# Kernel optimization log

Measured on AMD Instinct MI355X. Metric: run time of the kernel, lower is better.

## Reference

```python
import jax, jax.numpy as jnp
import numpy as np

C = 128          # hidden_channels
H = 8            # num_heads
D = C // H       # head dim = 16
OUT = 64         # out_channels
L = 2            # num_layers
NN = (30000, 60000, 6000)                 # poi, road, region node counts
NE = (200000, 300000, 200000, 100000)     # edges per edge type
ETS = ((0, 1), (1, 1), (1, 2), (2, 0))    # (src_type, dst_type) per edge type


def setup_inputs():
    key = jax.random.key(0)
    ks = iter(jax.random.split(key, 40))
    s = 1.0 / np.sqrt(C)
    sd = 1.0 / np.sqrt(D)
    inp = {}
    inp['x_poi'] = jax.random.normal(next(ks), (NN[0], C), jnp.float32)
    inp['x_road'] = jax.random.normal(next(ks), (NN[1], C), jnp.float32)
    inp['x_region'] = jax.random.normal(next(ks), (NN[2], C), jnp.float32)
    for et, (si, di) in enumerate(ETS):
        inp[f'e{et}_src'] = jax.random.randint(next(ks), (NE[et],), 0, NN[si], jnp.int32)
        inp[f'e{et}_dst'] = jax.random.randint(next(ks), (NE[et],), 0, NN[di], jnp.int32)
    # per-node-type input projection
    inp['lin_w'] = jax.random.normal(next(ks), (3, C, C), jnp.float32) * s
    inp['lin_b'] = jax.random.normal(next(ks), (3, C), jnp.float32) * 0.01
    # per-layer, per-node-type K/Q/V and output projections
    for nm in ('kw', 'qw', 'vw', 'aw'):
        inp[nm] = jax.random.normal(next(ks), (L, 3, C, C), jnp.float32) * s
    for nm in ('kb', 'qb', 'vb', 'ab'):
        inp[nm] = jax.random.normal(next(ks), (L, 3, C), jnp.float32) * 0.01
    # per-layer, per-edge-type relation matrices and priors
    inp['a_rel'] = jax.random.normal(next(ks), (L, 4, H, D, D), jnp.float32) * sd
    inp['m_rel'] = jax.random.normal(next(ks), (L, 4, H, D, D), jnp.float32) * sd
    inp['p_rel'] = jnp.ones((L, 4, H), jnp.float32)
    inp['skip'] = jnp.ones((L, 3), jnp.float32)
    inp['out_w'] = jax.random.normal(next(ks), (C, OUT), jnp.float32) * s
    inp['out_b'] = jnp.zeros((OUT,), jnp.float32)
    return inp


def _seg_softmax(alpha, dst, n):
    amax = jax.lax.stop_gradient(jax.ops.segment_max(alpha, dst, num_segments=n))
    ex = jnp.exp(alpha - amax[dst])
    den = jax.ops.segment_sum(ex, dst, num_segments=n)
    return ex / (den[dst] + 1e-16)


def _hgt_forward(xs, edges, lin_w, lin_b, kw, kb, qw, qb, vw, vb, aw, ab,
                 a_rel, m_rel, p_rel, skip, out_w, out_b):
    # per-node-type input linear + relu
    xs = [jax.nn.relu(xs[i] @ lin_w[i] + lin_b[i]) for i in range(3)]
    scale = 1.0 / np.sqrt(D)
    for l in range(L):
        k = [(xs[i] @ kw[l, i] + kb[l, i]).reshape(-1, H, D) for i in range(3)]
        q = [(xs[i] @ qw[l, i] + qb[l, i]).reshape(-1, H, D) for i in range(3)]
        v = [(xs[i] @ vw[l, i] + vb[l, i]).reshape(-1, H, D) for i in range(3)]
        agg = [jnp.zeros((NN[i], H, D), xs[i].dtype) for i in range(3)]
        for et, (si, di) in enumerate(ETS):
            src, dst = edges[et]
            n = NN[di]
            ke = jnp.einsum('ehd,hdf->ehf', k[si][src], a_rel[l, et])   # [E,H,D]
            alpha = jnp.einsum('ehd,ehd->eh', q[di][dst], ke) * p_rel[l, et] * scale
            alpha = _seg_softmax(alpha, dst, n)                          # [E,H]
            m = jnp.einsum('ehd,hdf->ehf', v[si][src], m_rel[l, et])    # [E,H,D]
            agg[di] = agg[di] + jax.ops.segment_sum(m * alpha[..., None], dst, num_segments=n)
        new_xs = []
        for i in range(3):
            o = jax.nn.gelu(agg[i].reshape(-1, C)) @ aw[l, i] + ab[l, i]
            beta = jax.nn.sigmoid(skip[l, i])
            o = beta * o + (1.0 - beta) * xs[i]
            new_xs.append(jax.nn.relu(o))  # HGT applies activation after each conv
        xs = new_xs
    return (xs[0] @ out_w + out_b, xs[1] @ out_w + out_b, xs[2] @ out_w + out_b)


def reference(x_poi, x_road, x_region,
              e0_src, e0_dst, e1_src, e1_dst, e2_src, e2_dst, e3_src, e3_dst,
              lin_w, lin_b, kw, kb, qw, qb, vw, vb, aw, ab,
              a_rel, m_rel, p_rel, skip, out_w, out_b):
    edges = ((e0_src, e0_dst), (e1_src, e1_dst), (e2_src, e2_dst), (e3_src, e3_dst))
    return _hgt_forward([x_poi, x_road, x_region], edges,
                        lin_w, lin_b, kw, kb, qw, qb, vw, vb, aw, ab,
                        a_rel, m_rel, p_rel, skip, out_w, out_b)
```

## Files before the change

kernel.cpp:

```cpp
#include <hip/hip_runtime.h>
#include <cstddef>
#include <cstdint>


typedef __attribute__((ext_vector_type(8))) short short8;
typedef __attribute__((ext_vector_type(4))) float floatx4;

__device__ __forceinline__ float gelu_fast(float x) {
    float u = 1.5957691216057308f * x * (1.0f + 0.044715f * x * x);
    return x / (1.0f + __expf(-u));
}

__device__ __forceinline__ unsigned short f2bf(float f) {
    unsigned u = __float_as_uint(f);
    u += 0x7fffu + ((u >> 16) & 1);
    return (unsigned short)(u >> 16);
}

__device__ __forceinline__ float bf2f(unsigned short h) {
    return __uint_as_float((unsigned)h << 16);
}

__device__ __forceinline__ void up8(uint4 u, float* f) {
    f[0] = __uint_as_float(u.x << 16); f[1] = __uint_as_float(u.x & 0xffff0000u);
    f[2] = __uint_as_float(u.y << 16); f[3] = __uint_as_float(u.y & 0xffff0000u);
    f[4] = __uint_as_float(u.z << 16); f[5] = __uint_as_float(u.z & 0xffff0000u);
    f[6] = __uint_as_float(u.w << 16); f[7] = __uint_as_float(u.w & 0xffff0000u);
}

__device__ __forceinline__ uint4 pk8(const float* f) {
    uint4 u;
    u.x = (unsigned)f2bf(f[0]) | ((unsigned)f2bf(f[1]) << 16);
    u.y = (unsigned)f2bf(f[2]) | ((unsigned)f2bf(f[3]) << 16);
    u.z = (unsigned)f2bf(f[4]) | ((unsigned)f2bf(f[5]) << 16);
    u.w = (unsigned)f2bf(f[6]) | ((unsigned)f2bf(f[7]) << 16);
    return u;
}

__global__ __launch_bounds__(256) void gemm_proj(
    const unsigned short* __restrict__ Abf,
    const unsigned short* __restrict__ Wt,
    const float* __restrict__ bias,
    unsigned short* __restrict__ outbf, int ldo, int Nrows, int cpb, int nct)
{
    const int wave = threadIdx.x >> 6, lane = threadIdx.x & 63;
    const int quad = lane >> 4, l16 = lane & 15;
    const int rowStart = (blockIdx.y * 4 + wave) * 32;
    if (rowStart >= Nrows) return;
    short8 Afr[2][4];
    #pragma unroll
    for (int rt = 0; rt < 2; ++rt) {
        int m = rowStart + rt * 16 + l16;
        const unsigned short* ap = Abf + (size_t)((m < Nrows) ? m : 0) * 128 + quad * 8;
        #pragma unroll
        for (int kc = 0; kc < 4; ++kc)
            Afr[rt][kc] = *(const short8*)(ap + kc * 32);
    }
    int ct1 = blockIdx.x * cpb + cpb;
    if (ct1 > nct) ct1 = nct;
    for (int ct = blockIdx.x * cpb; ct < ct1; ++ct) {
        int colBase = ct * 64;
        const unsigned short* wp = Wt + (size_t)(colBase + l16) * 128 + quad * 8;
        short8 B[4][4];
        #pragma unroll
        for (int c = 0; c < 4; ++c)
            #pragma unroll
            for (int kc = 0; kc < 4; ++kc)
                B[c][kc] = *(const short8*)(wp + (size_t)c * 2048 + kc * 32);
        floatx4 acc[2][4] = {{{0,0,0,0},{0,0,0,0},{0,0,0,0},{0,0,0,0}},
                             {{0,0,0,0},{0,0,0,0},{0,0,0,0},{0,0,0,0}}};
        #pragma unroll
        for (int kc = 0; kc < 4; ++kc)
            #pragma unroll
            for (int c = 0; c < 4; ++c) {
                acc[0][c] = __builtin_amdgcn_mfma_f32_16x16x32_bf16(Afr[0][kc], B[c][kc], acc[0][c], 0, 0, 0);
                acc[1][c] = __builtin_amdgcn_mfma_f32_16x16x32_bf16(Afr[1][kc], B[c][kc], acc[1][c], 0, 0, 0);
            }
        #pragma unroll
        for (int rt = 0; rt < 2; ++rt) {
            int row0 = rowStart + rt * 16 + quad * 4;
            #pragma unroll
            for (int c = 0; c < 4; ++c) {
                int col = colBase + c * 16 + l16;
                float bv = bias[col];
                #pragma unroll
                for (int r = 0; r < 4; ++r) {
                    int row = row0 + r;
                    if (row < Nrows)
                        outbf[(size_t)row * ldo + col] = f2bf(acc[rt][c][r] + bv);
                }
            }
        }
    }
}

template<bool AF32, bool GIN, bool SKIP>
__global__ __launch_bounds__(256) void gemm_node(
    const void* __restrict__ a0v, const void* __restrict__ a1v, const void* __restrict__ a2v,
    const unsigned short* __restrict__ WtB, const float* __restrict__ biasB,
    const unsigned short* __restrict__ xoldB, const float* __restrict__ skipB,
    unsigned short* __restrict__ outB)
{
    const int TN[3]   = {30000, 60000, 6000};
    const int TOFF[3] = {0, 30000, 90000};
    int by = blockIdx.x;
    int t  = (by < 469) ? 0 : (by < 1407) ? 1 : 2;
    int lb = by - ((t == 0) ? 0 : (t == 1) ? 469 : 1407);
    int Nrows = TN[t];
    const void* av = (t == 0) ? a0v : (t == 1) ? a1v : a2v;
    const unsigned short* Wt = WtB + (size_t)t * 16384;
    const float* bias = biasB + t * 128;
    const unsigned short* xold = xoldB + (size_t)TOFF[t] * 128;
    unsigned short* out = outB + (size_t)TOFF[t] * 128;
    const int wave = threadIdx.x >> 6, lane = threadIdx.x & 63;
    const int quad = lane >> 4, l16 = lane & 15;
    const int rowStart = (lb * 4 + wave) * 16;
    if (rowStart >= Nrows) return;
    int m = rowStart + l16;
    size_t base = (size_t)((m < Nrows) ? m : 0) * 128 + quad * 8;
    short8 Afr[4];
    #pragma unroll
    for (int kc = 0; kc < 4; ++kc) {
        if (AF32) {
            const float* ap = (const float*)av + base;
            float4 f0 = *(const float4*)(ap + kc * 32);
            float4 f1 = *(const float4*)(ap + kc * 32 + 4);
            float af[8] = {f0.x, f0.y, f0.z, f0.w, f1.x, f1.y, f1.z, f1.w};
            short8 a;
            #pragma unroll
            for (int i = 0; i < 8; ++i) a[i] = (short)f2bf(af[i]);
            Afr[kc] = a;
        } else if (GIN) {
            const unsigned short* ap = (const unsigned short*)av + base;
            short8 a8 = *(const short8*)(ap + kc * 32);
            short8 a;
            #pragma unroll
            for (int i = 0; i < 8; ++i)
                a[i] = (short)f2bf(gelu_fast(bf2f((unsigned short)a8[i])));
            Afr[kc] = a;
        } else {
            const unsigned short* ap = (const unsigned short*)av + base;
            Afr[kc] = *(const short8*)(ap + kc * 32);
        }
    }
    float beta = 0.f, omb = 0.f;
    if (SKIP) { beta = 1.0f / (1.0f + __expf(-skipB[t])); omb = 1.0f - beta; }
    int row0 = rowStart + quad * 4;
    #pragma unroll
    for (int ct = 0; ct < 2; ++ct) {
        int colBase = ct * 64;
        const unsigned short* wp = Wt + (size_t)(colBase + l16) * 128 + quad * 8;
        #pragma unroll
        for (int c = 0; c < 4; ++c) {
            floatx4 acc = {0, 0, 0, 0};
            #pragma unroll
            for (int kc = 0; kc < 4; ++kc) {
                short8 B = *(const short8*)(wp + (size_t)c * 2048 + kc * 32);
                acc = __builtin_amdgcn_mfma_f32_16x16x32_bf16(Afr[kc], B, acc, 0, 0, 0);
            }
            int col = colBase + c * 16 + l16;
            float bv = bias[col];
            #pragma unroll
            for (int r = 0; r < 4; ++r) {
                int row = row0 + r;
                if (row < Nrows) {
                    float o = acc[r] + bv;
                    if (SKIP) o = beta * o + omb * bf2f(xold[(size_t)row * 128 + col]);
                    o = fmaxf(o, 0.f);
                    out[(size_t)row * 128 + col] = f2bf(o);
                }
            }
        }
    }
}

__global__ __launch_bounds__(256) void gemm_out(
    const unsigned short* __restrict__ Abf,
    const unsigned short* __restrict__ Wt,
    const float* __restrict__ bias,
    float* __restrict__ out, int Nrows)
{
    const int wave = threadIdx.x >> 6, lane = threadIdx.x & 63;
    const int quad = lane >> 4, l16 = lane & 15;
    const int rowBase = (blockIdx.x * 4 + wave) * 16;
    if (rowBase >= Nrows) return;
    const unsigned short* wp = Wt + (size_t)l16 * 128 + quad * 8;
    int m = rowBase + l16;
    const unsigned short* ap = Abf + (size_t)((m < Nrows) ? m : 0) * 128 + quad * 8;
    short8 Afr[4];
    #pragma unroll
    for (int kc = 0; kc < 4; ++kc) Afr[kc] = *(const short8*)(ap + kc * 32);
    int row0 = rowBase + quad * 4;
    #pragma unroll
    for (int c = 0; c < 4; ++c) {
        floatx4 acc = {0, 0, 0, 0};
        #pragma unroll
        for (int kc = 0; kc < 4; ++kc) {
            short8 B = *(const short8*)(wp + (size_t)c * 2048 + kc * 32);
            acc = __builtin_amdgcn_mfma_f32_16x16x32_bf16(Afr[kc], B, acc, 0, 0, 0);
        }
        int col = c * 16 + l16;
        float bv = bias[col];
        #pragma unroll
        for (int r = 0; r < 4; ++r) {
            int row = row0 + r;
            if (row < Nrows)
                out[(size_t)row * 64 + col] = acc[r] + bv;
        }
    }
}

__global__ __launch_bounds__(128) void prep_qpack(
    const float* __restrict__ qw, const float* __restrict__ qb,
    unsigned short* __restrict__ Wpack, float* __restrict__ bpack)
{
    const int pre[3] = {0, 49152, 131072};
    const int preB[3] = {0, 384, 1024};
    int n = threadIdx.x, k = blockIdx.x, t = blockIdx.y, l = blockIdx.z;
    unsigned short* Wp = Wpack + (size_t)l * 180224 + pre[t];
    Wp[(size_t)n * 128 + k] = f2bf(qw[(size_t)(l * 3 + t) * 16384 + (size_t)k * 128 + n]);
    if (k == 0) bpack[l * 1408 + preB[t] + n] = qb[(l * 3 + t) * 128 + n];
}

__global__ __launch_bounds__(128) void fold_rel_pack(
    const float* __restrict__ kw, const float* __restrict__ kb,
    const float* __restrict__ vw, const float* __restrict__ vb,
    const float* __restrict__ a_rel, const float* __restrict__ m_rel,
    unsigned short* __restrict__ Wpack, float* __restrict__ bpack)
{
    const int SIv[4] = {0, 1, 1, 2};
    const int SLOT[4] = {0, 0, 1, 0};
    const int pre[3] = {0, 49152, 131072};
    const int preB[3] = {0, 384, 1024};
    int hf = threadIdx.x, h = hf >> 4, f = hf & 15;
    int c = blockIdx.x, et = blockIdx.y, l = blockIdx.z;
    int si = SIv[et];
    const float* kwp  = kw + (size_t)(l * 3 + si) * 16384;
    const float* vwp  = vw + (size_t)(l * 3 + si) * 16384;
    const float* kbp  = kb + (size_t)(l * 3 + si) * 128;
    const float* vbp  = vb + (size_t)(l * 3 + si) * 128;
    const float* arel = a_rel + (size_t)(l * 4 + et) * 2048;
    const float* mrel = m_rel + (size_t)(l * 4 + et) * 2048;
    float sk = 0.f, sv = 0.f;
    #pragma unroll
    for (int d = 0; d < 16; ++d) {
        float ar = arel[(h * 16 + d) * 16 + f];
        float mr = mrel[(h * 16 + d) * 16 + f];
        sk = fmaf(kwp[c * 128 + h * 16 + d], ar, sk);
        sv = fmaf(vwp[c * 128 + h * 16 + d], mr, sv);
    }
    int rowoff = 128 + 256 * SLOT[et];
    unsigned short* Wp = Wpack + (size_t)l * 180224 + pre[si];
    Wp[(size_t)(rowoff + hf) * 128 + c]       = f2bf(sk);
    Wp[(size_t)(rowoff + 128 + hf) * 128 + c] = f2bf(sv);
    if (c == 0) {
        float bk = 0.f, bvv = 0.f;
        #pragma unroll
        for (int d = 0; d < 16; ++d) {
            bk  = fmaf(kbp[h * 16 + d], arel[(h * 16 + d) * 16 + f], bk);
            bvv = fmaf(vbp[h * 16 + d], mrel[(h * 16 + d) * 16 + f], bvv);
        }
        float* bp = bpack + l * 1408 + preB[si];
        bp[rowoff + hf]       = bk;
        bp[rowoff + 128 + hf] = bvv;
    }
}

__global__ __launch_bounds__(128) void prep_w9(
    const float* __restrict__ lin_w, const float* __restrict__ aw,
    unsigned short* __restrict__ lwt, unsigned short* __restrict__ awt)
{
    int n = threadIdx.x, k = blockIdx.x, mi = blockIdx.y;
    const float* w; unsigned short* wt; int m;
    if (mi < 3) { w = lin_w; wt = lwt; m = mi; }
    else        { w = aw;    wt = awt; m = mi - 3; }
    wt[(size_t)m * 16384 + (size_t)n * 128 + k] =
        f2bf(w[(size_t)m * 16384 + (size_t)k * 128 + n]);
}

__global__ __launch_bounds__(64) void prep_owt(
    const float* __restrict__ ow, unsigned short* __restrict__ owt)
{
    int n = threadIdx.x, k = blockIdx.x;
    owt[(size_t)n * 128 + k] = f2bf(ow[(size_t)k * 64 + n]);
}

__global__ __launch_bounds__(256) void hist_all(
    const int* __restrict__ d0, const int* __restrict__ d1,
    const int* __restrict__ d2, const int* __restrict__ d3,
    int* __restrict__ deg4)
{
    const int Ev[4] = {200000, 300000, 200000, 100000};
    int et = blockIdx.y;
    int e = blockIdx.x * 256 + threadIdx.x;
    if (e >= Ev[et]) return;
    const int* d = et == 0 ? d0 : et == 1 ? d1 : et == 2 ? d2 : d3;
    atomicAdd(&deg4[et * 60000 + d[e]], 1);
}

__global__ __launch_bounds__(256) void scan_tile_all(
    const int* __restrict__ deg4,
    int* __restrict__ r0, int* __restrict__ r1, int* __restrict__ r2, int* __restrict__ r3,
    int* __restrict__ tsum4)
{
    const int Ndv[4] = {60000, 60000, 6000, 30000};
    __shared__ int ls[256];
    int et = blockIdx.y;
    int n = Ndv[et];
    const int* deg = deg4 + et * 60000;
    int* rowptr = et == 0 ? r0 : et == 1 ? r1 : et == 2 ? r2 : r3;
    int b = blockIdx.x, tid = threadIdx.x;
    int base = b * 1024 + tid * 4;
    int v0 = 0, v1 = 0, v2 = 0, v3 = 0;
    if (base + 3 < n) {
        int4 t = *(const int4*)(deg + base);
        v0 = t.x; v1 = t.y; v2 = t.z; v3 = t.w;
    } else {
        if (base + 0 < n) v0 = deg[base + 0];
        if (base + 1 < n) v1 = deg[base + 1];
        if (base + 2 < n) v2 = deg[base + 2];
        if (base + 3 < n) v3 = deg[base + 3];
    }
    int s = v0 + v1 + v2 + v3;
    ls[tid] = s;
    __syncthreads();
    #pragma unroll
    for (int off = 1; off < 256; off <<= 1) {
        int t = (tid >= off) ? ls[tid - off] : 0;
        __syncthreads();
        ls[tid] += t;
        __syncthreads();
    }
    int run = ls[tid] - s;
    int o0 = run; run += v0;
    int o1 = run; run += v1;
    int o2 = run; run += v2;
    int o3 = run;
    if (base + 3 < n) {
        *(int4*)(rowptr + base) = make_int4(o0, o1, o2, o3);
    } else {
        if (base + 0 < n) rowptr[base + 0] = o0;
        if (base + 1 < n) rowptr[base + 1] = o1;
        if (base + 2 < n) rowptr[base + 2] = o2;
    }
    if (tid == 255) tsum4[et * 64 + b] = ls[255];
}

__global__ __launch_bounds__(64) void scan_tsum_all(
    int* __restrict__ tsum4,
    int* __restrict__ r0, int* __restrict__ r1, int* __restrict__ r2, int* __restrict__ r3)
{
    const int Ndv[4] = {60000, 60000, 6000, 30000};
    int et = blockIdx.x;
    int n = Ndv[et];
    int nt = (n + 1023) >> 10;
    int* tileSum = tsum4 + et * 64;
    int* rowptr = et == 0 ? r0 : et == 1 ? r1 : et == 2 ? r2 : r3;
    int tid = threadIdx.x;
    int v = (tid < nt) ? tileSum[tid] : 0;
    int orig = v;
    #pragma unroll
    for (int off = 1; off < 64; off <<= 1) {
        int t = __shfl_up(v, off);
        if (tid >= off) v += t;
    }
    if (tid < nt) tileSum[tid] = v - orig;
    if (tid == nt - 1) rowptr[n] = v;
}

__global__ __launch_bounds__(256) void scan_add_all(
    int* __restrict__ r0, int* __restrict__ r1, int* __restrict__ r2, int* __restrict__ r3,
    const int* __restrict__ tsum4)
{
    const int Ndv[4] = {60000, 60000, 6000, 30000};
    int et = blockIdx.y;
    int n = Ndv[et];
    int* rowptr = et == 0 ? r0 : et == 1 ? r1 : et == 2 ? r2 : r3;
    int i = blockIdx.x * 256 + threadIdx.x;
    if (i < n) rowptr[i] += tsum4[et * 64 + (i >> 10)];
}

__global__ __launch_bounds__(256) void fill_all(
    const int* __restrict__ s0, const int* __restrict__ d0,
    const int* __restrict__ s1, const int* __restrict__ d1,
    const int* __restrict__ s2, const int* __restrict__ d2,
    const int* __restrict__ s3, const int* __restrict__ d3,
    const int* __restrict__ r0, const int* __restrict__ r1,
    const int* __restrict__ r2, const int* __restrict__ r3,
    int* __restrict__ deg4,
    int* __restrict__ c0, int* __restrict__ c1, int* __restrict__ c2, int* __restrict__ c3)
{
    const int Ev[4] = {200000, 300000, 200000, 100000};
    int et = blockIdx.y;
    int e = blockIdx.x * 256 + threadIdx.x;
    if (e >= Ev[et]) return;
    const int* src = et == 0 ? s0 : et == 1 ? s1 : et == 2 ? s2 : s3;
    const int* dst = et == 0 ? d0 : et == 1 ? d1 : et == 2 ? d2 : d3;
    const int* rowptr = et == 0 ? r0 : et == 1 ? r1 : et == 2 ? r2 : r3;
    int* csr = et == 0 ? c0 : et == 1 ? c1 : et == 2 ? c2 : c3;
    int d = dst[e];
    int pos = atomicAdd(&deg4[et * 60000 + d], 1);
    csr[rowptr[d] + pos] = src[e];
}

__device__ __forceinline__ void attn_run(
    const int* __restrict__ csr, int beg, int end,
    const unsigned short* __restrict__ kbase, int ld,
    const float* qf, float ph, float& m, float& l, float* o)
{
    if (beg >= end) return;
    int s = csr[beg];
    for (int j = beg; j < end; ++j) {
        int sn = (j + 1 < end) ? csr[j + 1] : 0;
        const uint4* kp = (const uint4*)(kbase + (size_t)s * ld);
        uint4 ku0 = kp[0], ku1 = kp[1];
        uint4 vu0 = kp[16], vu1 = kp[17];
        float kf[16], vf[16];
        up8(ku0, kf); up8(ku1, kf + 8);
        up8(vu0, vf); up8(vu1, vf + 8);
        float a = 0.f;
        #pragma unroll
        for (int i = 0; i < 16; ++i) a = fmaf(qf[i], kf[i], a);
        a *= ph;
        float mn = fmaxf(m, a);
        float sc = __expf(m - mn);
        float w  = __expf(a - mn);
        l = l * sc + w;
        #pragma unroll
        for (int i = 0; i < 16; ++i) o[i] = o[i] * sc + w * vf[i];
        m = mn; s = sn;
    }
}

__global__ __launch_bounds__(256) void agg_all(
    const int* __restrict__ rp0, const int* __restrict__ cs0,
    const int* __restrict__ rp1, const int* __restrict__ cs1,
    const int* __restrict__ rp2, const int* __restrict__ cs2,
    const int* __restrict__ rp3, const int* __restrict__ cs3,
    const unsigned short* __restrict__ P0, const unsigned short* __restrict__ P1,
    const unsigned short* __restrict__ P2,
    const float* __restrict__ prl,
    unsigned short* __restrict__ num)
{
    int gb = blockIdx.x, tid = threadIdx.x;
    float qf[16], o[16], r[16];
    if (gb < 1875) {
        int t = gb * 256 + tid;
        int node = t >> 3, h = t & 7;
        const uint4* qp = (const uint4*)(P1 + (size_t)node * 640 + h * 16);
        up8(qp[0], qf); up8(qp[1], qf + 8);
        float m0 = -INFINITY, l0 = 0.f;
        #pragma unroll
        for (int i = 0; i < 16; ++i) o[i] = 0.f;
        attn_run(cs0, rp0[node], rp0[node + 1], P0 + 128 + h * 16, 384,
                 qf, prl[h] * 0.25f, m0, l0, o);
        float i0 = 1.f / (l0 + 1e-16f);
        #pragma unroll
        for (int i = 0; i < 16; ++i) { r[i] = i0 * o[i]; o[i] = 0.f; }
        float m1 = -INFINITY, l1 = 0.f;
        attn_run(cs1, rp1[node], rp1[node + 1], P1 + 128 + h * 16, 640,
                 qf, prl[8 + h] * 0.25f, m1, l1, o);
        float i1 = 1.f / (l1 + 1e-16f);
        #pragma unroll
        for (int i = 0; i < 16; ++i) r[i] += i1 * o[i];
        uint4* np = (uint4*)(num + (size_t)(30000 + node) * 128 + h * 16);
        np[0] = pk8(r); np[1] = pk8(r + 8);
    } else if (gb < 2250) {
        int t = (gb - 1875) * 256 + tid;
        int node = t >> 4, h = t & 7, half = (t >> 3) & 1;
        int beg = rp2[node], end = rp2[node + 1];
        int mid = beg + ((end - beg + 1) >> 1);
        if (half == 0) end = mid; else beg = mid;
        const uint4* qp = (const uint4*)(P2 + (size_t)node * 384 + h * 16);
        up8(qp[0], qf); up8(qp[1], qf + 8);
        float m = -INFINITY, l = 0.f;
        #pragma unroll
        for (int i = 0; i < 16; ++i) o[i] = 0.f;
        attn_run(cs2, beg, end, P1 + 384 + h * 16, 640,
                 qf, prl[16 + h] * 0.25f, m, l, o);
        float mp = __shfl_xor(m, 8);
        float lp = __shfl_xor(l, 8);
        float mn = fmaxf(m, mp);
        float sc  = (l  > 0.f) ? __expf(m  - mn) : 0.f;
        float scp = (lp > 0.f) ? __expf(mp - mn) : 0.f;
        l = l * sc + lp * scp;
        #pragma unroll
        for (int i = 0; i < 16; ++i) {
            float op = __shfl_xor(o[i], 8);
            o[i] = o[i] * sc + op * scp;
        }
        if (half) return;
        float inv = 1.f / (l + 1e-16f);
        #pragma unroll
        for (int i = 0; i < 16; ++i) r[i] = inv * o[i];
        uint4* np = (uint4*)(num + (size_t)(90000 + node) * 128 + h * 16);
        np[0] = pk8(r); np[1] = pk8(r + 8);
    } else {
        int t = (gb - 2250) * 256 + tid;
        if (t >= 240000) return;
        int node = t >> 3, h = t & 7;
        const uint4* qp = (const uint4*)(P0 + (size_t)node * 384 + h * 16);
        up8(qp[0], qf); up8(qp[1], qf + 8);
        float m = -INFINITY, l = 0.f;
        #pragma unroll
        for (int i = 0; i < 16; ++i) o[i] = 0.f;
        attn_run(cs3, rp3[node], rp3[node + 1], P2 + 128 + h * 16, 384,
                 qf, prl[24 + h] * 0.25f, m, l, o);
        float inv = 1.f / (l + 1e-16f);
        #pragma unroll
        for (int i = 0; i < 16; ++i) r[i] = inv * o[i];
        uint4* np = (uint4*)(num + (size_t)node * 128 + h * 16);
        np[0] = pk8(r); np[1] = pk8(r + 8);
    }
}

extern "C" void kernel_launch(void* const* d_in, const int* in_sizes, int n_in,
                              void* d_out, int out_size, void* d_ws, size_t ws_size,
                              hipStream_t stream)
{
    (void)in_sizes; (void)n_in; (void)out_size; (void)ws_size;

    const float* xin[3] = {(const float*)d_in[0], (const float*)d_in[1], (const float*)d_in[2]};
    const int* esrc[4] = {(const int*)d_in[3], (const int*)d_in[5], (const int*)d_in[7], (const int*)d_in[9]};
    const int* edst[4] = {(const int*)d_in[4], (const int*)d_in[6], (const int*)d_in[8], (const int*)d_in[10]};
    const float* lin_w = (const float*)d_in[11];
    const float* lin_b = (const float*)d_in[12];
    const float* kw = (const float*)d_in[13];
    const float* qw = (const float*)d_in[14];
    const float* vw = (const float*)d_in[15];
    const float* aw = (const float*)d_in[16];
    const float* kb = (const float*)d_in[17];
    const float* qb = (const float*)d_in[18];
    const float* vb = (const float*)d_in[19];
    const float* ab = (const float*)d_in[20];
    const float* a_rel = (const float*)d_in[21];
    const float* m_rel = (const float*)d_in[22];
    const float* p_rel = (const float*)d_in[23];
    const float* skip  = (const float*)d_in[24];
    const float* out_w = (const float*)d_in[25];
    const float* out_b = (const float*)d_in[26];

    float* ws = (float*)d_ws;
    unsigned short* num   = (unsigned short*)ws;
    unsigned short* xs_bf = (unsigned short*)(ws + 6144000);
    unsigned short* proj  = (unsigned short*)(ws + 12288000);
    unsigned short* Wpack = (unsigned short*)(ws + 38400000);
    unsigned short* lwt   = (unsigned short*)(ws + 38580224);
    unsigned short* awt   = (unsigned short*)(ws + 38604800);
    unsigned short* owt   = (unsigned short*)(ws + 38653952);
    float*          bpack = ws + 38658048;
    int*            deg4  = (int*)(ws + 38660864);
    int*            tsum4 = (int*)(ws + 38900864);
    int* rp[4];
    rp[0] = (int*)(ws + 38901120);
    rp[1] = (int*)(ws + 38961128);
    rp[2] = (int*)(ws + 39021136);
    rp[3] = (int*)(ws + 39027144);
    int* cs[4];
    cs[0] = (int*)(ws + 39057152);
    cs[1] = (int*)(ws + 39257152);
    cs[2] = (int*)(ws + 39557152);
    cs[3] = (int*)(ws + 39757152);

    const int NNv[3] = {30000, 60000, 6000};
    const int OFF[3] = {0, 30000, 90000};
    const int NCOLS[3] = {384, 640, 384};
    unsigned short* P[3];
    P[0] = proj;
    P[1] = proj + (size_t)30000 * 384;
    P[2] = proj + (size_t)30000 * 384 + (size_t)60000 * 640;

    dim3 blk(256);

    hipMemsetAsync(deg4, 0, 960000, stream);
    hist_all<<<dim3(1172, 4), blk, 0, stream>>>(edst[0], edst[1], edst[2], edst[3], deg4);
    scan_tile_all<<<dim3(59, 4), blk, 0, stream>>>(deg4, rp[0], rp[1], rp[2], rp[3], tsum4);
    scan_tsum_all<<<dim3(4), dim3(64), 0, stream>>>(tsum4, rp[0], rp[1], rp[2], rp[3]);
    scan_add_all<<<dim3(235, 4), blk, 0, stream>>>(rp[0], rp[1], rp[2], rp[3], tsum4);
    hipMemsetAsync(deg4, 0, 960000, stream);
    fill_all<<<dim3(1172, 4), blk, 0, stream>>>(
        esrc[0], edst[0], esrc[1], edst[1], esrc[2], edst[2], esrc[3], edst[3],
        rp[0], rp[1], rp[2], rp[3], deg4, cs[0], cs[1], cs[2], cs[3]);

    prep_qpack<<<dim3(128, 3, 2), dim3(128), 0, stream>>>(qw, qb, Wpack, bpack);
    fold_rel_pack<<<dim3(128, 4, 2), dim3(128), 0, stream>>>(
        kw, kb, vw, vb, a_rel, m_rel, Wpack, bpack);
    prep_w9<<<dim3(128, 9), dim3(128), 0, stream>>>(lin_w, aw, lwt, awt);
    prep_owt<<<dim3(128), dim3(64), 0, stream>>>(out_w, owt);

    gemm_node<true, false, false><<<dim3(1501), blk, 0, stream>>>(
        xin[0], xin[1], xin[2], lwt, lin_b, nullptr, nullptr, xs_bf);

    for (int l = 0; l < 2; ++l) {
        const int CPB[3] = {3, 5, 2};
        const int XG[3]  = {2, 2, 3};
        for (int i = 0; i < 3; ++i) {
            dim3 g(XG[i], (NNv[i] + 127) / 128);
            gemm_proj<<<g, blk, 0, stream>>>(
                xs_bf + (size_t)OFF[i] * 128,
                Wpack + (size_t)l * 180224 + (i == 0 ? 0 : i == 1 ? 49152 : 131072),
                bpack + l * 1408 + (i == 0 ? 0 : i == 1 ? 384 : 1024),
                P[i], NCOLS[i], NNv[i], CPB[i], NCOLS[i] / 64);
        }

        agg_all<<<dim3(3188), blk, 0, stream>>>(
            rp[0], cs[0], rp[1], cs[1], rp[2], cs[2], rp[3], cs[3],
            P[0], P[1], P[2], p_rel + (size_t)l * 32, num);

        gemm_node<false, true, true><<<dim3(1501), blk, 0, stream>>>(
            num, num + (size_t)30000 * 128, num + (size_t)90000 * 128,
            awt + (size_t)l * 3 * 16384, ab + (size_t)l * 3 * 128,
            xs_bf, skip + l * 3, xs_bf);
    }

    gemm_out<<<dim3(1500), blk, 0, stream>>>(
        xs_bf, owt, out_b, (float*)d_out, 96000);
}
```

Measured before the change: 669.7 us.

## Fuse projection GEMMs, prefetch next edge, lazy softmax rescale, 4-way split region

The three per-node-type projection GEMM launches become one launch that maps block indices to node types. The attention inner loop now prefetches the next source row's K/V before computing the current edge. It also replaces the per-edge online-softmax rescale with a lazy rescale that only fires when the running max grows by more than 8. Region-destination aggregation is split four ways per node instead of two, merged with two shuffle rounds. These aim to cut launch overhead, hide gather latency and reduce exp work, at the cost of more registers and a lazy-max accuracy tradeoff.

```diff
diff --git a/kernel.cpp b/kernel.cpp
--- a/kernel.cpp
+++ b/kernel.cpp
@@ -37,15 +37,37 @@
     return u;
 }
 
-__global__ __launch_bounds__(256) void gemm_proj(
-    const unsigned short* __restrict__ Abf,
-    const unsigned short* __restrict__ Wt,
-    const float* __restrict__ bias,
-    unsigned short* __restrict__ outbf, int ldo, int Nrows, int cpb, int nct)
-{
+__global__ __launch_bounds__(256) void gemm_proj_all(
+    const unsigned short* __restrict__ xs_bf,
+    const unsigned short* __restrict__ Wl,
+    const float* __restrict__ bl,
+    unsigned short* __restrict__ proj)
+{
+    const int    NN_[3]  = {30000, 60000, 6000};
+    const int    OFFr[3] = {0, 30000, 90000};
+    const int    WOFF[3] = {0, 49152, 131072};
+    const int    BOFF[3] = {0, 384, 1024};
+    const size_t POFF[3] = {0, 11520000u, 49920000u};
+    const int    LDO[3]  = {384, 640, 384};
+    const int    CPBv[3] = {3, 5, 2};
+
+    int by = blockIdx.x, t, lb;
+    if (by < 938)       { t = 1; lb = by; }
+    else if (by < 1408) { t = 0; lb = by - 938; }
+    else                { t = 2; lb = by - 1408; }
+    int bx, byy;
+    if (t == 2) { byy = lb / 3; bx = lb - byy * 3; }
+    else        { bx = lb & 1; byy = lb >> 1; }
+
+    const unsigned short* Abf = xs_bf + (size_t)OFFr[t] * 128;
+    const unsigned short* Wt  = Wl + WOFF[t];
+    const float* bias = bl + BOFF[t];
+    unsigned short* outbf = proj + POFF[t];
+    const int ldo = LDO[t], Nrows = NN_[t], cpb = CPBv[t], nct = ldo >> 6;
+
     const int wave = threadIdx.x >> 6, lane = threadIdx.x & 63;
     const int quad = lane >> 4, l16 = lane & 15;
-    const int rowStart = (blockIdx.y * 4 + wave) * 32;
+    const int rowStart = (byy * 4 + wave) * 32;
     if (rowStart >= Nrows) return;
     short8 Afr[2][4];
     #pragma unroll
@@ -56,9 +78,9 @@
         for (int kc = 0; kc < 4; ++kc)
             Afr[rt][kc] = *(const short8*)(ap + kc * 32);
     }
-    int ct1 = blockIdx.x * cpb + cpb;
+    int ct1 = bx * cpb + cpb;
     if (ct1 > nct) ct1 = nct;
-    for (int ct = blockIdx.x * cpb; ct < ct1; ++ct) {
+    for (int ct = bx * cpb; ct < ct1; ++ct) {
         int colBase = ct * 64;
         const unsigned short* wp = Wt + (size_t)(colBase + l16) * 128 + quad * 8;
         short8 B[4][4];
@@ -410,11 +432,16 @@
 {
     if (beg >= end) return;
     int s = csr[beg];
+    const uint4* kp = (const uint4*)(kbase + (size_t)s * ld);
+    uint4 ku0 = kp[0], ku1 = kp[1];
+    uint4 vu0 = kp[16], vu1 = kp[17];
     for (int j = beg; j < end; ++j) {
-        int sn = (j + 1 < end) ? csr[j + 1] : 0;
-        const uint4* kp = (const uint4*)(kbase + (size_t)s * ld);
-        uint4 ku0 = kp[0], ku1 = kp[1];
-        uint4 vu0 = kp[16], vu1 = kp[17];
+        uint4 nk0 = ku0, nk1 = ku1, nv0 = vu0, nv1 = vu1;
+        if (j + 1 < end) {
+            int sn = csr[j + 1];
+            const uint4* np = (const uint4*)(kbase + (size_t)sn * ld);
+            nk0 = np[0]; nk1 = np[1]; nv0 = np[16]; nv1 = np[17];
+        }
         float kf[16], vf[16];
         up8(ku0, kf); up8(ku1, kf + 8);
         up8(vu0, vf); up8(vu1, vf + 8);
@@ -422,13 +449,19 @@
         #pragma unroll
         for (int i = 0; i < 16; ++i) a = fmaf(qf[i], kf[i], a);
         a *= ph;
-        float mn = fmaxf(m, a);
-        float sc = __expf(m - mn);
-        float w  = __expf(a - mn);
-        l = l * sc + w;
-        #pragma unroll
-        for (int i = 0; i < 16; ++i) o[i] = o[i] * sc + w * vf[i];
-        m = mn; s = sn;
+        float d = a - m;
+        if (d > 8.f) {
+            float sc = __expf(-d);
+            l *= sc;
+            #pragma unroll
+            for (int i = 0; i < 16; ++i) o[i] *= sc;
+            m = a; d = 0.f;
+        }
+        float w = __expf(d);
+        l += w;
+        #pragma unroll
+        for (int i = 0; i < 16; ++i) o[i] = fmaf(w, vf[i], o[i]);
+        ku0 = nk0; ku1 = nk1; vu0 = nv0; vu1 = nv1;
     }
 }
 
@@ -465,12 +498,13 @@
         for (int i = 0; i < 16; ++i) r[i] += i1 * o[i];
         uint4* np = (uint4*)(num + (size_t)(30000 + node) * 128 + h * 16);
         np[0] = pk8(r); np[1] = pk8(r + 8);
-    } else if (gb < 2250) {
+    } else if (gb < 2625) {
         int t = (gb - 1875) * 256 + tid;
-        int node = t >> 4, h = t & 7, half = (t >> 3) & 1;
-        int beg = rp2[node], end = rp2[node + 1];
-        int mid = beg + ((end - beg + 1) >> 1);
-        if (half == 0) end = mid; else beg = mid;
+        int node = t >> 5, h = t & 7, sub = (t >> 3) & 3;
+        int beg0 = rp2[node], end0 = rp2[node + 1];
+        int n = end0 - beg0;
+        int beg = beg0 + ((n * sub) >> 2);
+        int end = beg0 + ((n * (sub + 1)) >> 2);
         const uint4* qp = (const uint4*)(P2 + (size_t)node * 384 + h * 16);
         up8(qp[0], qf); up8(qp[1], qf + 8);
         float m = -INFINITY, l = 0.f;
@@ -478,25 +512,29 @@
         for (int i = 0; i < 16; ++i) o[i] = 0.f;
         attn_run(cs2, beg, end, P1 + 384 + h * 16, 640,
                  qf, prl[16 + h] * 0.25f, m, l, o);
-        float mp = __shfl_xor(m, 8);
-        float lp = __shfl_xor(l, 8);
-        float mn = fmaxf(m, mp);
-        float sc  = (l  > 0.f) ? __expf(m  - mn) : 0.f;
-        float scp = (lp > 0.f) ? __expf(mp - mn) : 0.f;
-        l = l * sc + lp * scp;
-        #pragma unroll
-        for (int i = 0; i < 16; ++i) {
-            float op = __shfl_xor(o[i], 8);
-            o[i] = o[i] * sc + op * scp;
-        }
-        if (half) return;
+        #pragma unroll
+        for (int st = 8; st <= 16; st <<= 1) {
+            float mp = __shfl_xor(m, st);
+            float lp = __shfl_xor(l, st);
+            float mn = fmaxf(m, mp);
+            float sc  = (l  > 0.f) ? __expf(m  - mn) : 0.f;
+            float scp = (lp > 0.f) ? __expf(mp - mn) : 0.f;
+            l = l * sc + lp * scp;
+            #pragma unroll
+            for (int i = 0; i < 16; ++i) {
+                float op = __shfl_xor(o[i], st);
+                o[i] = o[i] * sc + op * scp;
+            }
+            m = mn;
+        }
+        if (sub) return;
         float inv = 1.f / (l + 1e-16f);
         #pragma unroll
         for (int i = 0; i < 16; ++i) r[i] = inv * o[i];
         uint4* np = (uint4*)(num + (size_t)(90000 + node) * 128 + h * 16);
         np[0] = pk8(r); np[1] = pk8(r + 8);
     } else {
-        int t = (gb - 2250) * 256 + tid;
+        int t = (gb - 2625) * 256 + tid;
         if (t >= 240000) return;
         int node = t >> 3, h = t & 7;
         const uint4* qp = (const uint4*)(P0 + (size_t)node * 384 + h * 16);
@@ -562,9 +600,6 @@
     cs[2] = (int*)(ws + 39557152);
     cs[3] = (int*)(ws + 39757152);
 
-    const int NNv[3] = {30000, 60000, 6000};
-    const int OFF[3] = {0, 30000, 90000};
-    const int NCOLS[3] = {384, 640, 384};
     unsigned short* P[3];
     P[0] = proj;
     P[1] = proj + (size_t)30000 * 384;
@@ -592,18 +627,10 @@
         xin[0], xin[1], xin[2], lwt, lin_b, nullptr, nullptr, xs_bf);
 
     for (int l = 0; l < 2; ++l) {
-        const int CPB[3] = {3, 5, 2};
-        const int XG[3]  = {2, 2, 3};
-        for (int i = 0; i < 3; ++i) {
-            dim3 g(XG[i], (NNv[i] + 127) / 128);
-            gemm_proj<<<g, blk, 0, stream>>>(
-                xs_bf + (size_t)OFF[i] * 128,
-                Wpack + (size_t)l * 180224 + (i == 0 ? 0 : i == 1 ? 49152 : 131072),
-                bpack + l * 1408 + (i == 0 ? 0 : i == 1 ? 384 : 1024),
-                P[i], NCOLS[i], NNv[i], CPB[i], NCOLS[i] / 64);
-        }
-
-        agg_all<<<dim3(3188), blk, 0, stream>>>(
+        gemm_proj_all<<<dim3(1549), blk, 0, stream>>>(
+            xs_bf, Wpack + (size_t)l * 180224, bpack + l * 1408, proj);
+
+        agg_all<<<dim3(3563), blk, 0, stream>>>(
             rp[0], cs[0], rp[1], cs[1], rp[2], cs[2], rp[3], cs[3],
             P[0], P[1], P[2], p_rel + (size_t)l * 32, num);
 
```

Result: faster. 656.5 us (-2.0%).
